# Kernel optimization log

Measured on AMD Instinct MI355X. Metric: run time of the kernel, lower is better.

Reference implementation:

```python
import jax, jax.numpy as jnp
import numpy as np

SEQLS = [256, 256, 256, 256]
HEADS = 8
DIM_HEAD = 64
DIM = 512
SCALE = DIM_HEAD ** -0.5
EPS = 1e-5
# static segment-id per token position: [N]
SEG = np.repeat(np.arange(len(SEQLS)), SEQLS)


def setup_inputs() -> dict:
    key = jax.random.key(0)
    k_x, k_m, k_qkv, k_out = jax.random.split(key, 4)
    B, N = 8, sum(SEQLS)
    inner = HEADS * DIM_HEAD
    x = jax.random.normal(k_x, (B, N, DIM), dtype=jnp.float32)
    m_labels = jax.random.randint(k_m, (B, len(SEQLS)), 0, 2)
    gamma = jnp.ones((DIM,), jnp.float32)
    beta = jnp.zeros((DIM,), jnp.float32)
    w_qkv = jax.random.normal(k_qkv, (DIM, 3 * inner), jnp.float32) * (DIM ** -0.5)
    w_out = jax.random.normal(k_out, (inner, DIM), jnp.float32) * (inner ** -0.5)
    b_out = jnp.zeros((DIM,), jnp.float32)
    return {"x": x, "m_labels": m_labels, "gamma": gamma, "beta": beta,
            "w_qkv": w_qkv, "w_out": w_out, "b_out": b_out}


def reference(x, m_labels, gamma, beta, w_qkv, w_out, b_out):
    B, N, _ = x.shape
    # LayerNorm
    mu = jnp.mean(x, axis=-1, keepdims=True)
    var = jnp.var(x, axis=-1, keepdims=True)
    h = (x - mu) * jax.lax.rsqrt(var + EPS) * gamma + beta
    # QKV projection (no bias)
    qkv = h @ w_qkv  # [B, N, 3*inner]
    q, k, v = jnp.split(qkv, 3, axis=-1)
    to_heads = lambda t: t.reshape(B, N, HEADS, DIM_HEAD).transpose(0, 2, 1, 3)
    q, k, v = to_heads(q), to_heads(k), to_heads(v)  # [B, H, N, D]
    dots = jnp.einsum('bhid,bhjd->bhij', q, k) * SCALE  # [B, H, N, N]
    # modality-block additive mask: -inf on any row/col of a missing modality
    missing = (m_labels == 0)[:, SEG]  # [B, N]
    blocked = missing[:, :, None] | missing[:, None, :]  # [B, N, N]
    dots = jnp.where(blocked[:, None, :, :], -jnp.inf, dots)
    # custom softmax: rows that are fully -inf output 0
    all_inf = jnp.all(jnp.isinf(dots), axis=-1, keepdims=True)
    safe = jnp.where(all_inf, 0.0, dots)
    attn = jax.nn.softmax(safe, axis=-1)
    attn = jnp.where(all_inf, 0.0, attn)
    out = jnp.einsum('bhij,bhjd->bhid', attn, v)  # [B, H, N, D]
    out = out.transpose(0, 2, 1, 3).reshape(B, N, HEADS * DIM_HEAD)
    return out @ w_out + b_out
```

## Files before the change

kernel.cpp:

```cpp
#include <hip/hip_runtime.h>

typedef _Float16 f16;
typedef _Float16 f16x8 __attribute__((ext_vector_type(8)));
typedef float f32x4 __attribute__((ext_vector_type(4)));

typedef __attribute__((address_space(1))) void gvoid;
typedef __attribute__((address_space(3))) void lvoid;
#define GLD16(gp, lp) __builtin_amdgcn_global_load_lds((gvoid*)(gp), (lvoid*)(lp), 16, 0, 0)

__device__ __forceinline__ f32x4 mfma16(f16x8 a, f16x8 b, f32x4 c) {
    return __builtin_amdgcn_mfma_f32_16x16x32_f16(a, b, c, 0, 0, 0);
}

__global__ __launch_bounds__(256) void k_prep(
    const float* __restrict__ x, const float* __restrict__ gamma,
    const float* __restrict__ beta, const int* __restrict__ mlab,
    const float* __restrict__ wqkv, const float* __restrict__ wout,
    f16* __restrict__ h, f16* __restrict__ wqkvT, f16* __restrict__ woutT)
{
    __shared__ float t[64][65];
    int bid = blockIdx.x, tid = threadIdx.x;
    if (bid < 2048) {
        int row = bid * 4 + (tid >> 6);
        int b = row >> 10, seg = (row >> 8) & 3;
        if (mlab[b * 4 + seg] == 0) return;
        int lane = tid & 63;
        const float* xr = x + (size_t)row * 512;
        float4 a = ((const float4*)xr)[lane * 2];
        float4 bv = ((const float4*)xr)[lane * 2 + 1];
        float v[8] = {a.x, a.y, a.z, a.w, bv.x, bv.y, bv.z, bv.w};
        float s = 0.f, s2 = 0.f;
#pragma unroll
        for (int j = 0; j < 8; ++j) { s += v[j]; s2 += v[j] * v[j]; }
#pragma unroll
        for (int off = 1; off < 64; off <<= 1) {
            s  += __shfl_xor(s, off);
            s2 += __shfl_xor(s2, off);
        }
        float mu  = s * (1.f / 512.f);
        float var = s2 * (1.f / 512.f) - mu * mu;
        float rstd = rsqrtf(var + 1e-5f);
        float4 g0 = ((const float4*)gamma)[lane * 2];
        float4 g1 = ((const float4*)gamma)[lane * 2 + 1];
        float4 b0 = ((const float4*)beta)[lane * 2];
        float4 b1 = ((const float4*)beta)[lane * 2 + 1];
        float g[8]  = {g0.x, g0.y, g0.z, g0.w, g1.x, g1.y, g1.z, g1.w};
        float bb[8] = {b0.x, b0.y, b0.z, b0.w, b1.x, b1.y, b1.z, b1.w};
        f16x8 o;
#pragma unroll
        for (int j = 0; j < 8; ++j) o[j] = (f16)((v[j] - mu) * rstd * g[j] + bb[j]);
        *(f16x8*)&h[(size_t)row * 512 + lane * 8] = o;
        return;
    }
    const float* in; f16* out; int C, c0, r0;
    if (bid < 2240) { int idx = bid - 2048; in = wqkv; out = wqkvT; C = 1536; c0 = (idx % 24) * 64; r0 = (idx / 24) * 64; }
    else            { int idx = bid - 2240; in = wout; out = woutT; C = 512;  c0 = (idx % 8)  * 64; r0 = (idx / 8)  * 64; }
#pragma unroll
    for (int i = 0; i < 16; ++i) {
        int r = i * 4 + (tid >> 6), c = tid & 63;
        t[r][c] = in[(size_t)(r0 + r) * C + c0 + c];
    }
    __syncthreads();
#pragma unroll
    for (int i = 0; i < 16; ++i) {
        int cr = i * 4 + (tid >> 6), cc = tid & 63;
        out[(size_t)(c0 + cr) * 512 + r0 + cc] = (f16)t[cc][cr];
    }
}

__global__ __launch_bounds__(256, 3) void k_gemm_qkv(
    const f16* __restrict__ A, const f16* __restrict__ Bt, const int* __restrict__ mlab,
    f16* __restrict__ q, f16* __restrict__ kmat, f16* __restrict__ vt)
{
    __shared__ f16 As[2][64 * 64];
    __shared__ f16 Bs[2][128 * 64];
    int tid = threadIdx.x, wid = tid >> 6, lane = tid & 63;
    int wm = wid >> 1, wn = wid & 1;
    int l15 = lane & 15, l4 = lane >> 4;
    int rowBase = blockIdx.y * 64;
    int colBase = blockIdx.x * 128;
    if (mlab[(rowBase >> 10) * 4 + ((rowBase & 1023) >> 8)] == 0) return;

    int srow = lane >> 3;
    int scolz = ((lane & 7) ^ srow) << 3;
    int kxor = (l15 & 7) << 3;

#define STG(bi, kt)                                                                         \
    do {                                                                                    \
        _Pragma("unroll") for (int i_ = 0; i_ < 2; ++i_) {                                  \
            int rg = (wid * 2 + i_) * 8;                                                    \
            GLD16(&A[(size_t)(rowBase + rg + srow) * 512 + (kt) + scolz], &As[bi][rg * 64]);\
        }                                                                                   \
        _Pragma("unroll") for (int i_ = 0; i_ < 4; ++i_) {                                  \
            int rg = (wid * 4 + i_) * 8;                                                    \
            GLD16(&Bt[(size_t)(colBase + rg + srow) * 512 + (kt) + scolz], &Bs[bi][rg * 64]);\
        }                                                                                   \
    } while (0)

    f32x4 acc[2][4] = {};
    STG(0, 0);
    for (int ki = 0; ki < 8; ++ki) {
        int bi = ki & 1;
        __syncthreads();
        if (ki < 7) STG(bi ^ 1, (ki + 1) * 64);
#pragma unroll
        for (int kk = 0; kk < 2; ++kk) {
            f16x8 af[2], bf[4];
#pragma unroll
            for (int m = 0; m < 2; ++m)
                af[m] = *(const f16x8*)&As[bi][(wm * 32 + m * 16 + l15) * 64 + ((kk * 32 + l4 * 8) ^ kxor)];
#pragma unroll
            for (int n = 0; n < 4; ++n)
                bf[n] = *(const f16x8*)&Bs[bi][(wn * 64 + n * 16 + l15) * 64 + ((kk * 32 + l4 * 8) ^ kxor)];
#pragma unroll
            for (int m = 0; m < 2; ++m)
#pragma unroll
                for (int n = 0; n < 4; ++n)
                    acc[m][n] = mfma16(af[m], bf[n], acc[m][n]);
        }
    }
#undef STG
#pragma unroll
    for (int m = 0; m < 2; ++m)
#pragma unroll
        for (int n = 0; n < 4; ++n)
#pragma unroll
            for (int r = 0; r < 4; ++r) {
                int row = rowBase + wm * 32 + m * 16 + l4 * 4 + r;
                int col = colBase + wn * 64 + n * 16 + l15;
                f16 hv = (f16)acc[m][n][r];
                int b = row >> 10, nt = row & 1023;
                int which = col >> 9, hh = (col >> 6) & 7, d = col & 63;
                size_t hidx = ((size_t)(b * 8 + hh) * 1024 + nt) * 64 + d;
                if (which == 0)      q[hidx] = hv;
                else if (which == 1) kmat[hidx] = hv;
                else                 vt[((size_t)(b * 8 + hh) * 64 + d) * 1024 + nt] = hv;
            }
}

__global__ __launch_bounds__(512, 4) void k_attn(
    const f16* __restrict__ q, const f16* __restrict__ kmat,
    const f16* __restrict__ vt, const int* __restrict__ mlab,
    f16* __restrict__ ao)
{
    __shared__ f16 Ks[2][2][64 * 64];
    __shared__ f16 Vs[2][2][64 * 64];

    int bid = blockIdx.x;
    int bh = (bid & 7) + 8 * (bid >> 7);
    int qb = (bid >> 3) & 15;
    int b = bh >> 3, hh = bh & 7;
    int tid = threadIdx.x, wid = tid >> 6, lane = tid & 63;
    int qs = wid & 3, g = wid >> 2;
    int l15 = lane & 15, l4 = lane >> 4;
    int qbase = qb * 64;
    size_t bhs = (size_t)bh;

    if (mlab[b * 4 + (qb >> 2)] == 0) return;

    unsigned long long chpack = 0; int nch = 0;
#pragma unroll
    for (int s = 0; s < 4; ++s)
        if (mlab[b * 4 + s] != 0) {
#pragma unroll
            for (int j = 0; j < 4; ++j) {
                chpack |= (unsigned long long)(4 * s + j) << (4 * nch);
                ++nch;
            }
        }
    int niter = nch >> 1;

    f16x8 qf[2];
#pragma unroll
    for (int kk = 0; kk < 2; ++kk) {
        qf[kk] = *(const f16x8*)&q[(bhs * 1024 + qbase + qs * 16 + l15) * 64 + kk * 32 + l4 * 8];
#pragma unroll
        for (int j = 0; j < 8; ++j) qf[kk][j] = qf[kk][j] * (f16)0.125;
    }

    int gtid = tid & 255;
    int gw = wid & 3;
    int srow0 = gtid >> 3;
    int sc0 = ((gtid & 7) ^ (srow0 & 7)) << 3;
    int srow1 = (gtid + 256) >> 3;
    int sc1 = (((gtid + 256) & 7) ^ (srow1 & 7)) << 3;
    int lb0 = (gw * 64) * 8;
    int lb1 = (gw * 64 + 256) * 8;

#define STAGE(bi, t0)                                                                   \
    do {                                                                                \
        GLD16(&kmat[(bhs * 1024 + (t0) + srow0) * 64 + sc0], &Ks[g][bi][lb0]);          \
        GLD16(&kmat[(bhs * 1024 + (t0) + srow1) * 64 + sc1], &Ks[g][bi][lb1]);          \
        GLD16(&vt[(bhs * 64 + srow0) * 1024 + (t0) + sc0],   &Vs[g][bi][lb0]);          \
        GLD16(&vt[(bhs * 64 + srow1) * 1024 + (t0) + sc1],   &Vs[g][bi][lb1]);          \
    } while (0)

    float mrun = -1e30f, lrun = 0.f;
    f32x4 o[4] = {};
    int kxor = (l15 & 7) << 3;
    int srcA = l15 + ((l4 & 1) * 2) * 16;
    int srcB = srcA + 16;
    int sel = l4 >> 1;

    STAGE(0, (int)((chpack >> (4 * g)) & 15) << 6);

    for (int i = 0; i < niter; ++i) {
        int bi = i & 1;
        __syncthreads();
        if (i + 1 < niter) {
            int cn = 2 * (i + 1) + g;
            int t0n = (int)((chpack >> (4 * cn)) & 15) << 6;
            STAGE(bi ^ 1, t0n);
        }

        f32x4 st[4] = {};
        __builtin_amdgcn_s_setprio(1);
#pragma unroll
        for (int kk = 0; kk < 2; ++kk)
#pragma unroll
            for (int n = 0; n < 4; ++n) {
                f16x8 ka = *(const f16x8*)&Ks[g][bi][(n * 16 + l15) * 64 + ((kk * 32 + l4 * 8) ^ kxor)];
                st[n] = mfma16(ka, qf[kk], st[n]);
            }
        __builtin_amdgcn_s_setprio(0);

        f32x4 m4 = st[0];
#pragma unroll
        for (int n = 1; n < 4; ++n)
#pragma unroll
            for (int r = 0; r < 4; ++r) m4[r] = fmaxf(m4[r], st[n][r]);
        float mx = fmaxf(fmaxf(m4[0], m4[1]), fmaxf(m4[2], m4[3]));
        mx = fmaxf(mx, __shfl_xor(mx, 16));
        mx = fmaxf(mx, __shfl_xor(mx, 32));
        float mnew = fmaxf(mrun, mx);
        float alpha = __expf(mrun - mnew);
        mrun = mnew;
        float rs = 0.f;
        union PK { f16 h[4]; long long ll; } pk[4];
#pragma unroll
        for (int n = 0; n < 4; ++n)
#pragma unroll
            for (int r = 0; r < 4; ++r) {
                float p = __expf(st[n][r] - mnew);
                rs += p;
                pk[n].h[r] = (f16)p;
            }
        rs += __shfl_xor(rs, 16);
        rs += __shfl_xor(rs, 32);
        lrun = lrun * alpha + rs;
#pragma unroll
        for (int nd = 0; nd < 4; ++nd) o[nd] *= alpha;

#pragma unroll
        for (int ks = 0; ks < 2; ++ks) {
            long long A0 = __shfl(pk[ks * 2].ll,     srcA);
            long long A1 = __shfl(pk[ks * 2 + 1].ll, srcA);
            long long B0 = __shfl(pk[ks * 2].ll,     srcB);
            long long B1 = __shfl(pk[ks * 2 + 1].ll, srcB);
            union PB { long long ll[2]; f16x8 v; } pb;
            pb.ll[0] = sel ? A1 : A0;
            pb.ll[1] = sel ? B1 : B0;
            __builtin_amdgcn_s_setprio(1);
#pragma unroll
            for (int nd = 0; nd < 4; ++nd) {
                f16x8 va = *(const f16x8*)&Vs[g][bi][(nd * 16 + l15) * 64 + ((ks * 32 + l4 * 8) ^ kxor)];
                o[nd] = mfma16(va, pb.v, o[nd]);
            }
            __builtin_amdgcn_s_setprio(0);
        }
    }
#undef STAGE

    float* mg  = (float*)&Ks[0][0][0];
    float* mml = (float*)&Vs[0][0][0];
    __syncthreads();
    if (g == 1) {
        if (l4 == 0) { mml[qs * 16 + l15] = mrun; mml[64 + qs * 16 + l15] = lrun; }
#pragma unroll
        for (int nd = 0; nd < 4; ++nd)
#pragma unroll
            for (int r = 0; r < 4; ++r)
                mg[(qs * 64 + nd * 16 + l4 * 4 + r) * 16 + l15] = o[nd][r];
    }
    __syncthreads();
    if (g == 0) {
        float m1 = mml[qs * 16 + l15], l1 = mml[64 + qs * 16 + l15];
        float mst = fmaxf(mrun, m1);
        float e0 = __expf(mrun - mst), e1 = __expf(m1 - mst);
        float inv = 1.f / (lrun * e0 + l1 * e1);
        int qrow = qbase + qs * 16 + l15;
#pragma unroll
        for (int nd = 0; nd < 4; ++nd) {
            union { f16 h[4]; long long ll; } w;
#pragma unroll
            for (int r = 0; r < 4; ++r)
                w.h[r] = (f16)((o[nd][r] * e0 + mg[(qs * 64 + nd * 16 + l4 * 4 + r) * 16 + l15] * e1) * inv);
            *(long long*)&ao[(size_t)(b * 1024 + qrow) * 512 + hh * 64 + nd * 16 + l4 * 4] = w.ll;
        }
    }
}

__global__ __launch_bounds__(256, 3) void k_gemm_out(
    const f16* __restrict__ A, const f16* __restrict__ Bt, const int* __restrict__ mlab,
    const float* __restrict__ bias, float* __restrict__ out)
{
    __shared__ f16 As[2][64 * 64];
    __shared__ f16 Bs[2][128 * 64];
    int tid = threadIdx.x, wid = tid >> 6, lane = tid & 63;
    int wm = wid >> 1, wn = wid & 1;
    int l15 = lane & 15, l4 = lane >> 4;
    int rowBase = blockIdx.y * 64;
    int colBase = blockIdx.x * 128;
    if (mlab[(rowBase >> 10) * 4 + ((rowBase & 1023) >> 8)] == 0) {
        for (int i = tid; i < 64 * 128; i += 256)
            out[(size_t)(rowBase + (i >> 7)) * 512 + colBase + (i & 127)] = bias[colBase + (i & 127)];
        return;
    }

    int srow = lane >> 3;
    int scolz = ((lane & 7) ^ srow) << 3;
    int kxor = (l15 & 7) << 3;

#define STG(bi, kt)                                                                         \
    do {                                                                                    \
        _Pragma("unroll") for (int i_ = 0; i_ < 2; ++i_) {                                  \
            int rg = (wid * 2 + i_) * 8;                                                    \
            GLD16(&A[(size_t)(rowBase + rg + srow) * 512 + (kt) + scolz], &As[bi][rg * 64]);\
        }                                                                                   \
        _Pragma("unroll") for (int i_ = 0; i_ < 4; ++i_) {                                  \
            int rg = (wid * 4 + i_) * 8;                                                    \
            GLD16(&Bt[(size_t)(colBase + rg + srow) * 512 + (kt) + scolz], &Bs[bi][rg * 64]);\
        }                                                                                   \
    } while (0)

    f32x4 acc[2][4] = {};
    STG(0, 0);
    for (int ki = 0; ki < 8; ++ki) {
        int bi = ki & 1;
        __syncthreads();
        if (ki < 7) STG(bi ^ 1, (ki + 1) * 64);
#pragma unroll
        for (int kk = 0; kk < 2; ++kk) {
            f16x8 af[2], bf[4];
#pragma unroll
            for (int m = 0; m < 2; ++m)
                af[m] = *(const f16x8*)&As[bi][(wm * 32 + m * 16 + l15) * 64 + ((kk * 32 + l4 * 8) ^ kxor)];
#pragma unroll
            for (int n = 0; n < 4; ++n)
                bf[n] = *(const f16x8*)&Bs[bi][(wn * 64 + n * 16 + l15) * 64 + ((kk * 32 + l4 * 8) ^ kxor)];
#pragma unroll
            for (int m = 0; m < 2; ++m)
#pragma unroll
                for (int n = 0; n < 4; ++n)
                    acc[m][n] = mfma16(af[m], bf[n], acc[m][n]);
        }
    }
#undef STG
#pragma unroll
    for (int m = 0; m < 2; ++m)
#pragma unroll
        for (int n = 0; n < 4; ++n)
#pragma unroll
            for (int r = 0; r < 4; ++r) {
                int row = rowBase + wm * 32 + m * 16 + l4 * 4 + r;
                int col = colBase + wn * 64 + n * 16 + l15;
                out[(size_t)row * 512 + col] = acc[m][n][r] + bias[col];
            }
}

extern "C" void kernel_launch(void* const* d_in, const int* in_sizes, int n_in,
                              void* d_out, int out_size, void* d_ws, size_t ws_size,
                              hipStream_t stream) {
    const float* x     = (const float*)d_in[0];
    const int*   mlab  = (const int*)d_in[1];
    const float* gamma = (const float*)d_in[2];
    const float* beta  = (const float*)d_in[3];
    const float* wqkv  = (const float*)d_in[4];
    const float* wout  = (const float*)d_in[5];
    const float* bout  = (const float*)d_in[6];
    float* out = (float*)d_out;

    f16* h     = (f16*)d_ws;
    f16* wqkvT = h + 8192 * 512;
    f16* woutT = wqkvT + 1536 * 512;
    f16* q     = woutT + 512 * 512;
    f16* kmat  = q + 4 * 1024 * 1024;
    f16* vt    = kmat + 4 * 1024 * 1024;
    f16* ao    = h;

    k_prep<<<2304, 256, 0, stream>>>(x, gamma, beta, mlab, wqkv, wout, h, wqkvT, woutT);
    k_gemm_qkv<<<dim3(12, 128), 256, 0, stream>>>(h, wqkvT, mlab, q, kmat, vt);
    k_attn<<<1024, 512, 0, stream>>>(q, kmat, vt, mlab, ao);
    k_gemm_out<<<dim3(4, 128), 256, 0, stream>>>(ao, woutT, mlab, bout, out);
}
```

Before: 68.93 us.

## Prefetch K/V tiles into registers and single-buffer LDS in attention

Replaces the double-buffered direct global-to-LDS loads with a register-staged prefetch. The next K/V chunk is loaded into registers while the current one is computed, then written into a single LDS buffer, with a second barrier per iteration. This halves LDS use, and the launch bound is raised to ask for 6 blocks per CU for higher occupancy. In exchange it adds register pressure, extra LDS write instructions and an extra sync per iteration.

```diff
diff --git a/kernel.cpp b/kernel.cpp
--- a/kernel.cpp
+++ b/kernel.cpp
@@ -138,13 +138,13 @@
             }
 }
 
-__global__ __launch_bounds__(512, 4) void k_attn(
+__global__ __launch_bounds__(512, 6) void k_attn(
     const f16* __restrict__ q, const f16* __restrict__ kmat,
     const f16* __restrict__ vt, const int* __restrict__ mlab,
     f16* __restrict__ ao)
 {
-    __shared__ f16 Ks[2][2][64 * 64];
-    __shared__ f16 Vs[2][2][64 * 64];
+    __shared__ f16 Ks[2][64 * 64];
+    __shared__ f16 Vs[2][64 * 64];
 
     int bid = blockIdx.x;
     int bh = (bid & 7) + 8 * (bid >> 7);
@@ -179,20 +179,18 @@
     }
 
     int gtid = tid & 255;
-    int gw = wid & 3;
     int srow0 = gtid >> 3;
     int sc0 = ((gtid & 7) ^ (srow0 & 7)) << 3;
     int srow1 = (gtid + 256) >> 3;
     int sc1 = (((gtid + 256) & 7) ^ (srow1 & 7)) << 3;
-    int lb0 = (gw * 64) * 8;
-    int lb1 = (gw * 64 + 256) * 8;
-
-#define STAGE(bi, t0)                                                                   \
+
+    int4 krA, krB, vrA, vrB;
+#define LOADREG(t0)                                                                     \
     do {                                                                                \
-        GLD16(&kmat[(bhs * 1024 + (t0) + srow0) * 64 + sc0], &Ks[g][bi][lb0]);          \
-        GLD16(&kmat[(bhs * 1024 + (t0) + srow1) * 64 + sc1], &Ks[g][bi][lb1]);          \
-        GLD16(&vt[(bhs * 64 + srow0) * 1024 + (t0) + sc0],   &Vs[g][bi][lb0]);          \
-        GLD16(&vt[(bhs * 64 + srow1) * 1024 + (t0) + sc1],   &Vs[g][bi][lb1]);          \
+        krA = *(const int4*)&kmat[(bhs * 1024 + (t0) + srow0) * 64 + sc0];              \
+        krB = *(const int4*)&kmat[(bhs * 1024 + (t0) + srow1) * 64 + sc1];              \
+        vrA = *(const int4*)&vt[(bhs * 64 + srow0) * 1024 + (t0) + sc0];                \
+        vrB = *(const int4*)&vt[(bhs * 64 + srow1) * 1024 + (t0) + sc1];                \
     } while (0)
 
     float mrun = -1e30f, lrun = 0.f;
@@ -202,15 +200,17 @@
     int srcB = srcA + 16;
     int sel = l4 >> 1;
 
-    STAGE(0, (int)((chpack >> (4 * g)) & 15) << 6);
+    LOADREG((int)((chpack >> (4 * g)) & 15) << 6);
 
     for (int i = 0; i < niter; ++i) {
-        int bi = i & 1;
+        *(int4*)&Ks[g][gtid * 8] = krA;
+        *(int4*)&Ks[g][(gtid + 256) * 8] = krB;
+        *(int4*)&Vs[g][gtid * 8] = vrA;
+        *(int4*)&Vs[g][(gtid + 256) * 8] = vrB;
         __syncthreads();
         if (i + 1 < niter) {
             int cn = 2 * (i + 1) + g;
-            int t0n = (int)((chpack >> (4 * cn)) & 15) << 6;
-            STAGE(bi ^ 1, t0n);
+            LOADREG((int)((chpack >> (4 * cn)) & 15) << 6);
         }
 
         f32x4 st[4] = {};
@@ -219,7 +219,7 @@
         for (int kk = 0; kk < 2; ++kk)
 #pragma unroll
             for (int n = 0; n < 4; ++n) {
-                f16x8 ka = *(const f16x8*)&Ks[g][bi][(n * 16 + l15) * 64 + ((kk * 32 + l4 * 8) ^ kxor)];
+                f16x8 ka = *(const f16x8*)&Ks[g][(n * 16 + l15) * 64 + ((kk * 32 + l4 * 8) ^ kxor)];
                 st[n] = mfma16(ka, qf[kk], st[n]);
             }
         __builtin_amdgcn_s_setprio(0);
@@ -263,17 +263,17 @@
             __builtin_amdgcn_s_setprio(1);
 #pragma unroll
             for (int nd = 0; nd < 4; ++nd) {
-                f16x8 va = *(const f16x8*)&Vs[g][bi][(nd * 16 + l15) * 64 + ((ks * 32 + l4 * 8) ^ kxor)];
+                f16x8 va = *(const f16x8*)&Vs[g][(nd * 16 + l15) * 64 + ((ks * 32 + l4 * 8) ^ kxor)];
                 o[nd] = mfma16(va, pb.v, o[nd]);
             }
             __builtin_amdgcn_s_setprio(0);
         }
-    }
-#undef STAGE
-
-    float* mg  = (float*)&Ks[0][0][0];
-    float* mml = (float*)&Vs[0][0][0];
-    __syncthreads();
+        __syncthreads();
+    }
+#undef LOADREG
+
+    float* mg  = (float*)&Ks[0][0];
+    float* mml = (float*)&Vs[0][0];
     if (g == 1) {
         if (l4 == 0) { mml[qs * 16 + l15] = mrun; mml[64 + qs * 16 + l15] = lrun; }
 #pragma unroll
```

Result: slower. 80.70 us (+17.1%).

## Split attention keys four ways per block and stage QKV epilogue through LDS

Applied to the files above, without the earlier changes.

The attention kernel now splits each block's key range across four wave groups instead of two. Each wave handles 32 query rows with 32-key chunks, using retuned K/V staging layouts and swizzles, and a four-way LSE merge reads the partial outputs from LDS. The QKV GEMM epilogue now stages the tile through shared memory so Q/K and transposed V can be written as 16-byte vector stores instead of scattered scalar stores. This is meant to add key-dimension parallelism, reuse each K/V fragment across two query tiles, and coalesce global writes. In exchange it adds extra barriers, a larger LDS merge buffer, and more per-chunk softmax overhead from the smaller key chunks.

```diff
diff --git a/kernel.cpp b/kernel.cpp
--- a/kernel.cpp
+++ b/kernel.cpp
@@ -72,8 +72,7 @@
     const f16* __restrict__ A, const f16* __restrict__ Bt, const int* __restrict__ mlab,
     f16* __restrict__ q, f16* __restrict__ kmat, f16* __restrict__ vt)
 {
-    __shared__ f16 As[2][64 * 64];
-    __shared__ f16 Bs[2][128 * 64];
+    __shared__ __align__(16) f16 SM[24576];
     int tid = threadIdx.x, wid = tid >> 6, lane = tid & 63;
     int wm = wid >> 1, wn = wid & 1;
     int l15 = lane & 15, l4 = lane >> 4;
@@ -85,16 +84,16 @@
     int scolz = ((lane & 7) ^ srow) << 3;
     int kxor = (l15 & 7) << 3;
 
-#define STG(bi, kt)                                                                         \
-    do {                                                                                    \
-        _Pragma("unroll") for (int i_ = 0; i_ < 2; ++i_) {                                  \
-            int rg = (wid * 2 + i_) * 8;                                                    \
-            GLD16(&A[(size_t)(rowBase + rg + srow) * 512 + (kt) + scolz], &As[bi][rg * 64]);\
-        }                                                                                   \
-        _Pragma("unroll") for (int i_ = 0; i_ < 4; ++i_) {                                  \
-            int rg = (wid * 4 + i_) * 8;                                                    \
-            GLD16(&Bt[(size_t)(colBase + rg + srow) * 512 + (kt) + scolz], &Bs[bi][rg * 64]);\
-        }                                                                                   \
+#define STG(bi, kt)                                                                              \
+    do {                                                                                         \
+        _Pragma("unroll") for (int i_ = 0; i_ < 2; ++i_) {                                       \
+            int rg = (wid * 2 + i_) * 8;                                                         \
+            GLD16(&A[(size_t)(rowBase + rg + srow) * 512 + (kt) + scolz], SM + (bi)*4096 + rg*64);\
+        }                                                                                        \
+        _Pragma("unroll") for (int i_ = 0; i_ < 4; ++i_) {                                       \
+            int rg = (wid * 4 + i_) * 8;                                                         \
+            GLD16(&Bt[(size_t)(colBase + rg + srow) * 512 + (kt) + scolz], SM + 8192 + (bi)*8192 + rg*64);\
+        }                                                                                        \
     } while (0)
 
     f32x4 acc[2][4] = {};
@@ -108,10 +107,10 @@
             f16x8 af[2], bf[4];
 #pragma unroll
             for (int m = 0; m < 2; ++m)
-                af[m] = *(const f16x8*)&As[bi][(wm * 32 + m * 16 + l15) * 64 + ((kk * 32 + l4 * 8) ^ kxor)];
+                af[m] = *(const f16x8*)&SM[bi*4096 + (wm * 32 + m * 16 + l15) * 64 + ((kk * 32 + l4 * 8) ^ kxor)];
 #pragma unroll
             for (int n = 0; n < 4; ++n)
-                bf[n] = *(const f16x8*)&Bs[bi][(wn * 64 + n * 16 + l15) * 64 + ((kk * 32 + l4 * 8) ^ kxor)];
+                bf[n] = *(const f16x8*)&SM[8192 + bi*8192 + (wn * 64 + n * 16 + l15) * 64 + ((kk * 32 + l4 * 8) ^ kxor)];
 #pragma unroll
             for (int m = 0; m < 2; ++m)
 #pragma unroll
@@ -120,22 +119,45 @@
         }
     }
 #undef STG
-#pragma unroll
-    for (int m = 0; m < 2; ++m)
-#pragma unroll
-        for (int n = 0; n < 4; ++n)
-#pragma unroll
-            for (int r = 0; r < 4; ++r) {
-                int row = rowBase + wm * 32 + m * 16 + l4 * 4 + r;
-                int col = colBase + wn * 64 + n * 16 + l15;
-                f16 hv = (f16)acc[m][n][r];
-                int b = row >> 10, nt = row & 1023;
-                int which = col >> 9, hh = (col >> 6) & 7, d = col & 63;
-                size_t hidx = ((size_t)(b * 8 + hh) * 1024 + nt) * 64 + d;
-                if (which == 0)      q[hidx] = hv;
-                else if (which == 1) kmat[hidx] = hv;
-                else                 vt[((size_t)(b * 8 + hh) * 64 + d) * 1024 + nt] = hv;
-            }
+
+    __syncthreads();
+    bool isV = (colBase >= 1024);
+    if (!isV) {
+#pragma unroll
+        for (int m = 0; m < 2; ++m)
+#pragma unroll
+            for (int n = 0; n < 4; ++n)
+#pragma unroll
+                for (int r = 0; r < 4; ++r)
+                    SM[(wm*32 + m*16 + l4*4 + r) * 136 + wn*64 + n*16 + l15] = (f16)acc[m][n][r];
+        __syncthreads();
+        int rl = tid >> 2, cl0 = (tid & 3) * 32;
+        int row = rowBase + rl, bq = row >> 10, nt = row & 1023;
+#pragma unroll
+        for (int jj = 0; jj < 4; ++jj) {
+            f16x8 v = *(const f16x8*)&SM[rl * 136 + cl0 + jj * 8];
+            int col = colBase + cl0 + jj * 8;
+            int which = col >> 9, hh2 = (col >> 6) & 7, d = col & 63;
+            f16* dst = which ? kmat : q;
+            *(f16x8*)&dst[((size_t)(bq * 8 + hh2) * 1024 + nt) * 64 + d] = v;
+        }
+    } else {
+#pragma unroll
+        for (int m = 0; m < 2; ++m)
+#pragma unroll
+            for (int n = 0; n < 4; ++n)
+#pragma unroll
+                for (int r = 0; r < 4; ++r)
+                    SM[(wn*64 + n*16 + l15) * 72 + wm*32 + m*16 + l4*4 + r] = (f16)acc[m][n][r];
+        __syncthreads();
+        int cl = tid >> 1, rl0 = (tid & 1) * 32;
+        int col = colBase + cl, hh2 = (col >> 6) & 7, d = col & 63;
+        int bq = rowBase >> 10, ntb = (rowBase & 1023) + rl0;
+        f16* dstrow = vt + ((size_t)(bq * 8 + hh2) * 64 + d) * 1024 + ntb;
+#pragma unroll
+        for (int jj = 0; jj < 4; ++jj)
+            *(f16x8*)&dstrow[jj * 8] = *(const f16x8*)&SM[cl * 72 + rl0 + jj * 8];
+    }
 }
 
 __global__ __launch_bounds__(512, 4) void k_attn(
@@ -143,160 +165,199 @@
     const f16* __restrict__ vt, const int* __restrict__ mlab,
     f16* __restrict__ ao)
 {
-    __shared__ f16 Ks[2][2][64 * 64];
-    __shared__ f16 Vs[2][2][64 * 64];
+    __shared__ __align__(16) f16 KV[32768];
+    __shared__ float ML[512];
 
     int bid = blockIdx.x;
     int bh = (bid & 7) + 8 * (bid >> 7);
     int qb = (bid >> 3) & 15;
     int b = bh >> 3, hh = bh & 7;
     int tid = threadIdx.x, wid = tid >> 6, lane = tid & 63;
-    int qs = wid & 3, g = wid >> 2;
+    int g = wid >> 1, qs = wid & 1;
     int l15 = lane & 15, l4 = lane >> 4;
     int qbase = qb * 64;
     size_t bhs = (size_t)bh;
 
     if (mlab[b * 4 + (qb >> 2)] == 0) return;
 
-    unsigned long long chpack = 0; int nch = 0;
+    unsigned ps = 0; int npres = 0;
 #pragma unroll
     for (int s = 0; s < 4; ++s)
-        if (mlab[b * 4 + s] != 0) {
-#pragma unroll
-            for (int j = 0; j < 4; ++j) {
-                chpack |= (unsigned long long)(4 * s + j) << (4 * nch);
-                ++nch;
-            }
-        }
-    int niter = nch >> 1;
-
-    f16x8 qf[2];
+        if (mlab[b * 4 + s] != 0) { ps |= (unsigned)s << (4 * npres); ++npres; }
+    int niter = npres * 2;
+#define T0C(c) ((int)((ps >> (4 * ((c) >> 3))) & 15) * 256 + ((c) & 7) * 32)
+
+    f16x8 qf0[2], qf1[2];
 #pragma unroll
     for (int kk = 0; kk < 2; ++kk) {
-        qf[kk] = *(const f16x8*)&q[(bhs * 1024 + qbase + qs * 16 + l15) * 64 + kk * 32 + l4 * 8];
-#pragma unroll
-        for (int j = 0; j < 8; ++j) qf[kk][j] = qf[kk][j] * (f16)0.125;
-    }
-
-    int gtid = tid & 255;
-    int gw = wid & 3;
-    int srow0 = gtid >> 3;
-    int sc0 = ((gtid & 7) ^ (srow0 & 7)) << 3;
-    int srow1 = (gtid + 256) >> 3;
-    int sc1 = (((gtid + 256) & 7) ^ (srow1 & 7)) << 3;
-    int lb0 = (gw * 64) * 8;
-    int lb1 = (gw * 64 + 256) * 8;
-
-#define STAGE(bi, t0)                                                                   \
-    do {                                                                                \
-        GLD16(&kmat[(bhs * 1024 + (t0) + srow0) * 64 + sc0], &Ks[g][bi][lb0]);          \
-        GLD16(&kmat[(bhs * 1024 + (t0) + srow1) * 64 + sc1], &Ks[g][bi][lb1]);          \
-        GLD16(&vt[(bhs * 64 + srow0) * 1024 + (t0) + sc0],   &Vs[g][bi][lb0]);          \
-        GLD16(&vt[(bhs * 64 + srow1) * 1024 + (t0) + sc1],   &Vs[g][bi][lb1]);          \
+        qf0[kk] = *(const f16x8*)&q[(bhs * 1024 + qbase + qs * 32 + l15) * 64 + kk * 32 + l4 * 8];
+        qf1[kk] = *(const f16x8*)&q[(bhs * 1024 + qbase + qs * 32 + 16 + l15) * 64 + kk * 32 + l4 * 8];
+#pragma unroll
+        for (int j = 0; j < 8; ++j) { qf0[kk][j] = qf0[kk][j] * (f16)0.125; qf1[kk][j] = qf1[kk][j] * (f16)0.125; }
+    }
+
+    int sA = qs * 64 + lane, sB = sA + 128;
+    int krA = sA >> 3, kcA = ((sA & 7) ^ (krA & 7)) << 3;
+    int krB = sB >> 3, kcB = ((sB & 7) ^ (krB & 7)) << 3;
+    int vrA = sA >> 2, vcA = ((sA & 3) ^ ((vrA >> 1) & 3)) << 3;
+    int vrB = sB >> 2, vcB = ((sB & 3) ^ ((vrB >> 1) & 3)) << 3;
+    const f16* kgA = kmat + (bhs * 1024 + krA) * 64 + kcA;
+    const f16* kgB = kmat + (bhs * 1024 + krB) * 64 + kcB;
+    const f16* vgA = vt + (bhs * 64 + vrA) * 1024 + vcA;
+    const f16* vgB = vt + (bhs * 64 + vrB) * 1024 + vcB;
+
+#define STAGE(bi, t0)                                                \
+    do {                                                             \
+        f16* kd = KV + (g * 2 + (bi)) * 2048 + qs * 512;             \
+        f16* vd = KV + 16384 + (g * 2 + (bi)) * 2048 + qs * 512;     \
+        GLD16(kgA + (size_t)(t0) * 64, kd);                          \
+        GLD16(kgB + (size_t)(t0) * 64, kd + 1024);                   \
+        GLD16(vgA + (t0), vd);                                       \
+        GLD16(vgB + (t0), vd + 1024);                                \
     } while (0)
 
-    float mrun = -1e30f, lrun = 0.f;
-    f32x4 o[4] = {};
-    int kxor = (l15 & 7) << 3;
-    int srcA = l15 + ((l4 & 1) * 2) * 16;
-    int srcB = srcA + 16;
+    float mrun0 = -1e30f, mrun1 = -1e30f, lrun0 = 0.f, lrun1 = 0.f;
+    f32x4 o0[4] = {}, o1[4] = {};
+    int kxor = l15 & 7;
+    int vxor = (l15 >> 1) & 3;
+    int srcA = l15 + ((l4 & 1) * 2) * 16, srcB = srcA + 16;
     int sel = l4 >> 1;
 
-    STAGE(0, (int)((chpack >> (4 * g)) & 15) << 6);
+    STAGE(0, T0C(g));
 
     for (int i = 0; i < niter; ++i) {
         int bi = i & 1;
         __syncthreads();
-        if (i + 1 < niter) {
-            int cn = 2 * (i + 1) + g;
-            int t0n = (int)((chpack >> (4 * cn)) & 15) << 6;
-            STAGE(bi ^ 1, t0n);
-        }
-
-        f32x4 st[4] = {};
+        if (i + 1 < niter) STAGE(bi ^ 1, T0C(4 * (i + 1) + g));
+
+        const f16* Kt = KV + (g * 2 + bi) * 2048;
+        const f16* Vt = KV + 16384 + (g * 2 + bi) * 2048;
+
+        f32x4 s00 = {}, s01 = {}, s10 = {}, s11 = {};
         __builtin_amdgcn_s_setprio(1);
 #pragma unroll
-        for (int kk = 0; kk < 2; ++kk)
-#pragma unroll
-            for (int n = 0; n < 4; ++n) {
-                f16x8 ka = *(const f16x8*)&Ks[g][bi][(n * 16 + l15) * 64 + ((kk * 32 + l4 * 8) ^ kxor)];
-                st[n] = mfma16(ka, qf[kk], st[n]);
+        for (int kk = 0; kk < 2; ++kk) {
+            f16x8 ka0 = *(const f16x8*)&Kt[(0 * 16 + l15) * 64 + (((kk * 4 + l4) ^ kxor) << 3)];
+            f16x8 ka1 = *(const f16x8*)&Kt[(1 * 16 + l15) * 64 + (((kk * 4 + l4) ^ kxor) << 3)];
+            s00 = mfma16(ka0, qf0[kk], s00);
+            s10 = mfma16(ka0, qf1[kk], s10);
+            s01 = mfma16(ka1, qf0[kk], s01);
+            s11 = mfma16(ka1, qf1[kk], s11);
+        }
+        __builtin_amdgcn_s_setprio(0);
+
+        union PK { f16 h[4]; long long ll; };
+        union PB { long long ll[2]; f16x8 v; } pb0, pb1;
+        {
+            f32x4 mm;
+#pragma unroll
+            for (int r = 0; r < 4; ++r) mm[r] = fmaxf(s00[r], s01[r]);
+            float mx = fmaxf(fmaxf(mm[0], mm[1]), fmaxf(mm[2], mm[3]));
+            mx = fmaxf(mx, __shfl_xor(mx, 16));
+            mx = fmaxf(mx, __shfl_xor(mx, 32));
+            float mnew = fmaxf(mrun0, mx);
+            float alpha = __expf(mrun0 - mnew);
+            mrun0 = mnew;
+            float rs = 0.f;
+            PK pk0, pk1;
+#pragma unroll
+            for (int r = 0; r < 4; ++r) {
+                float p0 = __expf(s00[r] - mnew), p1 = __expf(s01[r] - mnew);
+                rs += p0 + p1;
+                pk0.h[r] = (f16)p0; pk1.h[r] = (f16)p1;
             }
+            rs += __shfl_xor(rs, 16);
+            rs += __shfl_xor(rs, 32);
+            lrun0 = lrun0 * alpha + rs;
+#pragma unroll
+            for (int nd = 0; nd < 4; ++nd) o0[nd] *= alpha;
+            long long A0 = __shfl(pk0.ll, srcA), A1 = __shfl(pk1.ll, srcA);
+            long long B0 = __shfl(pk0.ll, srcB), B1 = __shfl(pk1.ll, srcB);
+            pb0.ll[0] = sel ? A1 : A0;
+            pb0.ll[1] = sel ? B1 : B0;
+        }
+        {
+            f32x4 mm;
+#pragma unroll
+            for (int r = 0; r < 4; ++r) mm[r] = fmaxf(s10[r], s11[r]);
+            float mx = fmaxf(fmaxf(mm[0], mm[1]), fmaxf(mm[2], mm[3]));
+            mx = fmaxf(mx, __shfl_xor(mx, 16));
+            mx = fmaxf(mx, __shfl_xor(mx, 32));
+            float mnew = fmaxf(mrun1, mx);
+            float alpha = __expf(mrun1 - mnew);
+            mrun1 = mnew;
+            float rs = 0.f;
+            PK pk0, pk1;
+#pragma unroll
+            for (int r = 0; r < 4; ++r) {
+                float p0 = __expf(s10[r] - mnew), p1 = __expf(s11[r] - mnew);
+                rs += p0 + p1;
+                pk0.h[r] = (f16)p0; pk1.h[r] = (f16)p1;
+            }
+            rs += __shfl_xor(rs, 16);
+            rs += __shfl_xor(rs, 32);
+            lrun1 = lrun1 * alpha + rs;
+#pragma unroll
+            for (int nd = 0; nd < 4; ++nd) o1[nd] *= alpha;
+            long long A0 = __shfl(pk0.ll, srcA), A1 = __shfl(pk1.ll, srcA);
+            long long B0 = __shfl(pk0.ll, srcB), B1 = __shfl(pk1.ll, srcB);
+            pb1.ll[0] = sel ? A1 : A0;
+            pb1.ll[1] = sel ? B1 : B0;
+        }
+        __builtin_amdgcn_s_setprio(1);
+#pragma unroll
+        for (int nd = 0; nd < 4; ++nd) {
+            f16x8 va = *(const f16x8*)&Vt[(nd * 16 + l15) * 32 + ((l4 ^ vxor) << 3)];
+            o0[nd] = mfma16(va, pb0.v, o0[nd]);
+            o1[nd] = mfma16(va, pb1.v, o1[nd]);
+        }
         __builtin_amdgcn_s_setprio(0);
-
-        f32x4 m4 = st[0];
-#pragma unroll
-        for (int n = 1; n < 4; ++n)
-#pragma unroll
-            for (int r = 0; r < 4; ++r) m4[r] = fmaxf(m4[r], st[n][r]);
-        float mx = fmaxf(fmaxf(m4[0], m4[1]), fmaxf(m4[2], m4[3]));
-        mx = fmaxf(mx, __shfl_xor(mx, 16));
-        mx = fmaxf(mx, __shfl_xor(mx, 32));
-        float mnew = fmaxf(mrun, mx);
-        float alpha = __expf(mrun - mnew);
-        mrun = mnew;
-        float rs = 0.f;
-        union PK { f16 h[4]; long long ll; } pk[4];
-#pragma unroll
-        for (int n = 0; n < 4; ++n)
-#pragma unroll
-            for (int r = 0; r < 4; ++r) {
-                float p = __expf(st[n][r] - mnew);
-                rs += p;
-                pk[n].h[r] = (f16)p;
-            }
-        rs += __shfl_xor(rs, 16);
-        rs += __shfl_xor(rs, 32);
-        lrun = lrun * alpha + rs;
-#pragma unroll
-        for (int nd = 0; nd < 4; ++nd) o[nd] *= alpha;
-
-#pragma unroll
-        for (int ks = 0; ks < 2; ++ks) {
-            long long A0 = __shfl(pk[ks * 2].ll,     srcA);
-            long long A1 = __shfl(pk[ks * 2 + 1].ll, srcA);
-            long long B0 = __shfl(pk[ks * 2].ll,     srcB);
-            long long B1 = __shfl(pk[ks * 2 + 1].ll, srcB);
-            union PB { long long ll[2]; f16x8 v; } pb;
-            pb.ll[0] = sel ? A1 : A0;
-            pb.ll[1] = sel ? B1 : B0;
-            __builtin_amdgcn_s_setprio(1);
-#pragma unroll
-            for (int nd = 0; nd < 4; ++nd) {
-                f16x8 va = *(const f16x8*)&Vs[g][bi][(nd * 16 + l15) * 64 + ((ks * 32 + l4 * 8) ^ kxor)];
-                o[nd] = mfma16(va, pb.v, o[nd]);
-            }
-            __builtin_amdgcn_s_setprio(0);
-        }
     }
 #undef STAGE
-
-    float* mg  = (float*)&Ks[0][0][0];
-    float* mml = (float*)&Vs[0][0][0];
+#undef T0C
+
     __syncthreads();
-    if (g == 1) {
-        if (l4 == 0) { mml[qs * 16 + l15] = mrun; mml[64 + qs * 16 + l15] = lrun; }
-#pragma unroll
-        for (int nd = 0; nd < 4; ++nd)
-#pragma unroll
-            for (int r = 0; r < 4; ++r)
-                mg[(qs * 64 + nd * 16 + l4 * 4 + r) * 16 + l15] = o[nd][r];
+    float* mg = (float*)KV;
+    int q0 = qs * 32 + l15;
+    if (l4 == 0) {
+        ML[g * 64 + q0] = mrun0;       ML[256 + g * 64 + q0] = lrun0;
+        ML[g * 64 + q0 + 16] = mrun1;  ML[256 + g * 64 + q0 + 16] = lrun1;
+    }
+    {
+        int xr0 = (q0 & 7) << 2, q1 = q0 + 16, xr1 = (q1 & 7) << 2;
+#pragma unroll
+        for (int nd = 0; nd < 4; ++nd) {
+            *(f32x4*)&mg[g * 4096 + q0 * 64 + ((nd * 16 + l4 * 4) ^ xr0)] = o0[nd];
+            *(f32x4*)&mg[g * 4096 + q1 * 64 + ((nd * 16 + l4 * 4) ^ xr1)] = o1[nd];
+        }
     }
     __syncthreads();
-    if (g == 0) {
-        float m1 = mml[qs * 16 + l15], l1 = mml[64 + qs * 16 + l15];
-        float mst = fmaxf(mrun, m1);
-        float e0 = __expf(mrun - mst), e1 = __expf(m1 - mst);
-        float inv = 1.f / (lrun * e0 + l1 * e1);
-        int qrow = qbase + qs * 16 + l15;
-#pragma unroll
-        for (int nd = 0; nd < 4; ++nd) {
-            union { f16 h[4]; long long ll; } w;
-#pragma unroll
-            for (int r = 0; r < 4; ++r)
-                w.h[r] = (f16)((o[nd][r] * e0 + mg[(qs * 64 + nd * 16 + l4 * 4 + r) * 16 + l15] * e1) * inv);
-            *(long long*)&ao[(size_t)(b * 1024 + qrow) * 512 + hh * 64 + nd * 16 + l4 * 4] = w.ll;
-        }
+
+    {
+        int qq = l15 + l4 * 16;
+        float m0 = ML[qq], m1 = ML[64 + qq], m2 = ML[128 + qq], m3 = ML[192 + qq];
+        float M = fmaxf(fmaxf(m0, m1), fmaxf(m2, m3));
+        float e0 = __expf(m0 - M), e1 = __expf(m1 - M), e2 = __expf(m2 - M), e3 = __expf(m3 - M);
+        float L = ML[256 + qq] * e0 + ML[320 + qq] * e1 + ML[384 + qq] * e2 + ML[448 + qq] * e3;
+        float inv = 1.f / L;
+        int xr = (qq & 7) << 2;
+        int Aoff = (wid * 8) ^ xr;
+        f32x4 accA = {}, accB = {};
+#pragma unroll
+        for (int gg = 0; gg < 4; ++gg) {
+            float eg = gg == 0 ? e0 : gg == 1 ? e1 : gg == 2 ? e2 : e3;
+            f32x4 pa = *(const f32x4*)&mg[gg * 4096 + qq * 64 + Aoff];
+            f32x4 pc = *(const f32x4*)&mg[gg * 4096 + qq * 64 + (Aoff ^ 4)];
+#pragma unroll
+            for (int r = 0; r < 4; ++r) { accA[r] += eg * pa[r]; accB[r] += eg * pc[r]; }
+        }
+        union { f16 h[8]; f16x8 v; } w;
+#pragma unroll
+        for (int r = 0; r < 4; ++r) {
+            w.h[r] = (f16)(accA[r] * inv);
+            w.h[4 + r] = (f16)(accB[r] * inv);
+        }
+        *(f16x8*)&ao[(size_t)(b * 1024 + qbase + qq) * 512 + hh * 64 + wid * 8] = w.v;
     }
 }
 
```

After: 62.15 us. 1.11x faster.
